# Kernel tuning notes

Measured on AMD Instinct MI355X. Metric: run time of the kernel, lower is better.

Reference implementation:

```python
import jax, jax.numpy as jnp
import numpy as np
import math

EPS = 1e-3          # self.eps
M = 0.5             # margin
H = 0.333           # rad_h
S = 64.0            # scale
HEAD_B = 0.5        # head_b
BATCH_MEAN = 0.0    # registered buffer initial value
BATCH_STD = 100.0   # registered buffer initial value
B, D, C = 1024, 512, 51332


def setup_inputs() -> dict:
    key = jax.random.key(0)
    k1, k2, k3, k4 = jax.random.split(key, 4)
    emb = jax.random.normal(k1, (B, D), dtype=jnp.float32)
    # face embeddings are typically l2-normalized before this head
    emb = emb / jnp.clip(jnp.linalg.norm(emb, axis=1, keepdims=True), 1e-5)
    # feature norms in a realistic range [5, 35)
    norms = jax.random.uniform(k2, (B, 1), dtype=jnp.float32) * 30.0 + 5.0
    kernel = jax.random.normal(k3, (D, C), dtype=jnp.float32)
    label = jax.random.randint(k4, (B,), 0, C)
    return {"embbedings": emb, "norms": norms, "kernel": kernel, "label": label}


def reference(embbedings, norms, kernel, label):
    # l2_norm(kernel, axis=0)
    kn = kernel / jnp.clip(jnp.linalg.norm(kernel, axis=0, keepdims=True), 1e-5)
    # [B, C] cosine logits
    cosine = jnp.clip(embbedings @ kn, -1.0 + EPS, 1.0 - EPS)
    # detached norm-based margin scaler ('batchnorm' branch)
    safe_norms = jax.lax.stop_gradient(jnp.clip(norms, 1e-3, 100.0))
    ms = jnp.clip((safe_norms - BATCH_MEAN) / (BATCH_STD + EPS) * H, -1.0, 1.0)[:, 0]  # [B]
    rows = jnp.arange(cosine.shape[0])
    # additive angular margin only at the label column (equivalent to the one-hot scatter)
    theta = jnp.arccos(cosine).at[rows, label].add(M * ms)
    cos_m = jnp.cos(jnp.clip(theta, EPS, math.pi - EPS))
    # subtractive cosine margin at the label column
    cos_m = cos_m.at[rows, label].add(-(HEAD_B - M * ms))
    return cos_m * S
```

## Files before the change

kernel.cpp:

```cpp
#include <hip/hip_runtime.h>
#include <hip/hip_bf16.h>
#include <math.h>

#define B_ROWS 1024
#define DDIM   512
#define CN     51332
#define CPAD   51456
#define EPSF   1e-3f
#define SCALE  64.0f

typedef unsigned short ushort_t;
typedef short bf16x8 __attribute__((ext_vector_type(8)));
typedef float f32x4  __attribute__((ext_vector_type(4)));
typedef unsigned short us8 __attribute__((ext_vector_type(8)));
typedef unsigned short us4 __attribute__((ext_vector_type(4)));

static __device__ __forceinline__ unsigned short f2bf(float f) {
    unsigned int u = __float_as_uint(f);
    u += 0x7fffu + ((u >> 16) & 1u);
    return (unsigned short)(u >> 16);
}

__global__ void colpass(const float* __restrict__ kern, ushort_t* __restrict__ kbT,
                        float* __restrict__ partials) {
    const int c  = blockIdx.x * 256 + threadIdx.x;
    const int dc = blockIdx.y;
    const int d0 = dc * 128;
    const bool valid = (c < CN);
    float s = 0.f;
    for (int d = d0; d < d0 + 128; d += 8) {
        us8 pk;
#pragma unroll
        for (int j = 0; j < 8; ++j) {
            float v = valid ? kern[(size_t)(d + j) * CN + c] : 0.f;
            s += v * v;
            pk[j] = f2bf(v);
        }
        *(us8*)&kbT[(size_t)c * DDIM + d] = pk;
    }
    partials[(size_t)dc * CPAD + c] = s;
}

__global__ void finnorm(const float* __restrict__ partials, float* __restrict__ inv_norm) {
    const int c = blockIdx.x * 256 + threadIdx.x;
    float s = partials[c] + partials[CPAD + c] + partials[2 * CPAD + c] + partials[3 * CPAD + c];
    inv_norm[c] = 1.0f / fmaxf(sqrtf(s), 1e-5f);
}

__global__ void embcast(const float* __restrict__ emb, ushort_t* __restrict__ embb) {
    const int t = blockIdx.x * 256 + threadIdx.x;
    const float4 v = ((const float4*)emb)[t];
    us4 o; o[0] = f2bf(v.x); o[1] = f2bf(v.y); o[2] = f2bf(v.z); o[3] = f2bf(v.w);
    *(us4*)&embb[(size_t)t * 4] = o;
}

__global__ __launch_bounds__(256) void gemm_kernel(
        const ushort_t* __restrict__ embb, const ushort_t* __restrict__ kbT,
        const float* __restrict__ inv_norm, float* __restrict__ out) {
    __shared__ ushort_t As[128 * 64];
    __shared__ ushort_t Bs[128 * 64];
    const int tid  = threadIdx.x;
    const int lane = tid & 63;
    const int wave = tid >> 6;
    const int wm = wave & 1, wn = wave >> 1;
    const int m0 = blockIdx.x * 128;
    const int n0 = blockIdx.y * 128;
    const int r8 = lane >> 3, c8 = lane & 7;
    const int lm = lane & 15;
    const int lq = lane >> 4;

    f32x4 acc[4][4];
#pragma unroll
    for (int i = 0; i < 4; ++i)
#pragma unroll
        for (int j = 0; j < 4; ++j)
            acc[i][j] = (f32x4){0.f, 0.f, 0.f, 0.f};

    for (int kt = 0; kt < 8; ++kt) {
        const int k0 = kt * 64;
#pragma unroll
        for (int it = 0; it < 4; ++it) {
            const int row = wave * 32 + it * 8;
            const ushort_t* gA = embb + (size_t)(m0 + row + r8) * DDIM + k0 + c8 * 8;
            __builtin_amdgcn_global_load_lds((__attribute__((address_space(1))) void*)gA,
                (__attribute__((address_space(3))) void*)&As[row * 64], 16, 0, 0);
            const ushort_t* gB = kbT + (size_t)(n0 + row + r8) * DDIM + k0 + c8 * 8;
            __builtin_amdgcn_global_load_lds((__attribute__((address_space(1))) void*)gB,
                (__attribute__((address_space(3))) void*)&Bs[row * 64], 16, 0, 0);
        }
        __syncthreads();
#pragma unroll
        for (int ks = 0; ks < 64; ks += 32) {
            bf16x8 a[4], b[4];
#pragma unroll
            for (int i = 0; i < 4; ++i)
                a[i] = *(const bf16x8*)&As[(wm * 64 + i * 16 + lm) * 64 + ks + lq * 8];
#pragma unroll
            for (int j = 0; j < 4; ++j)
                b[j] = *(const bf16x8*)&Bs[(wn * 64 + j * 16 + lm) * 64 + ks + lq * 8];
#pragma unroll
            for (int i = 0; i < 4; ++i)
#pragma unroll
                for (int j = 0; j < 4; ++j)
                    acc[i][j] = __builtin_amdgcn_mfma_f32_16x16x32_bf16(a[i], b[j], acc[i][j], 0, 0, 0);
        }
        __syncthreads();
    }

#pragma unroll
    for (int j = 0; j < 4; ++j) {
        const int col = n0 + wn * 64 + j * 16 + lm;
        const bool ok = col < CN;
        const float inv = ok ? inv_norm[col] : 0.f;
#pragma unroll
        for (int i = 0; i < 4; ++i) {
            const int row0 = m0 + wm * 64 + i * 16 + lq * 4;
#pragma unroll
            for (int r = 0; r < 4; ++r) {
                float v = acc[i][j][r] * inv;
                v = fminf(fmaxf(v, -(1.0f - EPSF)), 1.0f - EPSF) * SCALE;
                if (ok) out[(size_t)(row0 + r) * CN + col] = v;
            }
        }
    }
}

__global__ void fixup(const float* __restrict__ norms, const int* __restrict__ label,
                      float* __restrict__ out) {
    const int b = blockIdx.x * 256 + threadIdx.x;
    if (b >= B_ROWS) return;
    const int c = label[b];
    const float safe = fminf(fmaxf(norms[b], 1e-3f), 100.0f);
    const float ms = fminf(fmaxf(safe / (100.0f + 1e-3f) * 0.333f, -1.0f), 1.0f);
    const size_t idx = (size_t)b * CN + c;
    const float cosv = out[idx] * (1.0f / SCALE);
    float theta = acosf(cosv) + 0.5f * ms;
    theta = fminf(fmaxf(theta, EPSF), 3.14159265358979f - EPSF);
    out[idx] = (cosf(theta) - (0.5f - 0.5f * ms)) * SCALE;
}

extern "C" void kernel_launch(void* const* d_in, const int* in_sizes, int n_in,
                              void* d_out, int out_size, void* d_ws, size_t ws_size,
                              hipStream_t stream) {
    const float* emb   = (const float*)d_in[0];
    const float* norms = (const float*)d_in[1];
    const float* kern  = (const float*)d_in[2];
    const int*   label = (const int*)d_in[3];
    float* out = (float*)d_out;

    char* ws = (char*)d_ws;
    ushort_t* kbT = (ushort_t*)ws;
    size_t off = (size_t)CPAD * DDIM * 2;
    ushort_t* embb = (ushort_t*)(ws + off); off += (size_t)B_ROWS * DDIM * 2;
    float* inv_norm = (float*)(ws + off);   off += (size_t)CPAD * 4;
    float* partials = (float*)(ws + off);

    colpass<<<dim3(CPAD / 256, 4), 256, 0, stream>>>(kern, kbT, partials);
    embcast<<<dim3((B_ROWS * DDIM / 4) / 256), 256, 0, stream>>>(emb, embb);
    finnorm<<<dim3(CPAD / 256), 256, 0, stream>>>(partials, inv_norm);
    gemm_kernel<<<dim3(B_ROWS / 128, CPAD / 128), 256, 0, stream>>>(embb, kbT, inv_norm, out);
    fixup<<<dim3(B_ROWS / 256), 256, 0, stream>>>(norms, label, out);
}
```

Measured before the change: 477.8 us.

## Stage GEMM epilogue through LDS for coalesced stores and swizzle blocks per XCD

The GEMM epilogue now writes clamped, scaled results into the reused shared-memory buffer, one 64-row half at a time, with a rotation swizzle to avoid bank conflicts. It then reads them back and issues row-contiguous float4 global stores. The old path wrote scattered scalar stores to the very large output. The launch also becomes a 1D grid whose block index is remapped so that the 8 M-tiles sharing one kernel column tile land on the same XCD, improving L2 reuse of the bf16 weight tile. The cost is extra barriers and LDS traffic in the epilogue.

After: 455.7 us. 1.05x faster.

```diff
diff --git a/kernel.cpp b/kernel.cpp
--- a/kernel.cpp
+++ b/kernel.cpp
@@ -57,14 +57,20 @@
 __global__ __launch_bounds__(256) void gemm_kernel(
         const ushort_t* __restrict__ embb, const ushort_t* __restrict__ kbT,
         const float* __restrict__ inv_norm, float* __restrict__ out) {
-    __shared__ ushort_t As[128 * 64];
-    __shared__ ushort_t Bs[128 * 64];
+    __shared__ ushort_t smem[2 * 128 * 64];
+    ushort_t* As = smem;
+    ushort_t* Bs = smem + 128 * 64;
+    float*    Es = (float*)smem;
+
+    const int bid = blockIdx.x;
+    const int u   = (bid & 7) * 402 + (bid >> 3);
+    const int m0  = (u & 7) * 128;
+    const int n0  = (u >> 3) * 128;
+
     const int tid  = threadIdx.x;
     const int lane = tid & 63;
     const int wave = tid >> 6;
     const int wm = wave & 1, wn = wave >> 1;
-    const int m0 = blockIdx.x * 128;
-    const int n0 = blockIdx.y * 128;
     const int r8 = lane >> 3, c8 = lane & 7;
     const int lm = lane & 15;
     const int lq = lane >> 4;
@@ -107,19 +113,47 @@
         __syncthreads();
     }
 
+    float invn[4];
 #pragma unroll
     for (int j = 0; j < 4; ++j) {
         const int col = n0 + wn * 64 + j * 16 + lm;
-        const bool ok = col < CN;
-        const float inv = ok ? inv_norm[col] : 0.f;
+        invn[j] = (col < CN) ? inv_norm[col] : 0.f;
+    }
+
 #pragma unroll
-        for (int i = 0; i < 4; ++i) {
-            const int row0 = m0 + wm * 64 + i * 16 + lq * 4;
+    for (int half = 0; half < 2; ++half) {
+        __syncthreads();
+        if (wm == half) {
 #pragma unroll
-            for (int r = 0; r < 4; ++r) {
-                float v = acc[i][j][r] * inv;
-                v = fminf(fmaxf(v, -(1.0f - EPSF)), 1.0f - EPSF) * SCALE;
-                if (ok) out[(size_t)(row0 + r) * CN + col] = v;
+            for (int i = 0; i < 4; ++i)
+#pragma unroll
+                for (int j = 0; j < 4; ++j)
+#pragma unroll
+                    for (int r = 0; r < 4; ++r) {
+                        const int row = i * 16 + lq * 4 + r;
+                        const int col = wn * 64 + j * 16 + lm;
+                        const int cs  = (col + row * 4) & 127;
+                        float v = acc[i][j][r] * invn[j];
+                        v = fminf(fmaxf(v, -(1.0f - EPSF)), 1.0f - EPSF) * SCALE;
+                        Es[row * 128 + cs] = v;
+                    }
+        }
+        __syncthreads();
+#pragma unroll
+        for (int it = 0; it < 8; ++it) {
+            const int row = wave * 16 + it * 2 + (lane >> 5);
+            const int uq  = lane & 31;
+            const int us_ = (uq + row) & 31;
+            const f32x4 v = *(const f32x4*)&Es[row * 128 + us_ * 4];
+            const int grow = m0 + half * 64 + row;
+            const int gcol = n0 + uq * 4;
+            float* p = &out[(size_t)grow * CN + gcol];
+            if (gcol + 3 < CN) {
+                *(f32x4*)p = v;
+            } else {
+#pragma unroll
+                for (int e = 0; e < 4; ++e)
+                    if (gcol + e < CN) p[e] = v[e];
             }
         }
     }
@@ -158,6 +192,6 @@
     colpass<<<dim3(CPAD / 256, 4), 256, 0, stream>>>(kern, kbT, partials);
     embcast<<<dim3((B_ROWS * DDIM / 4) / 256), 256, 0, stream>>>(emb, embb);
     finnorm<<<dim3(CPAD / 256), 256, 0, stream>>>(partials, inv_norm);
-    gemm_kernel<<<dim3(B_ROWS / 128, CPAD / 128), 256, 0, stream>>>(embb, kbT, inv_norm, out);
+    gemm_kernel<<<dim3(3216), 256, 0, stream>>>(embb, kbT, inv_norm, out);
     fixup<<<dim3(B_ROWS / 256), 256, 0, stream>>>(norms, label, out);
 }
```
